# Performance work log

Hardware: AMD Instinct MI355X
Metric: run time of the kernel (lower is better)

The kernel has to match this reference:

```python
import jax, jax.numpy as jnp
import numpy as np

N_NODES = 128   # input_series_dim (nodes per graph)
FEAT = 512      # input_series_length
HID = 512       # hidden_channels
OUT = 10        # output_dimension
BATCH = 512     # batch_size


def setup_inputs() -> dict:
    key = jax.random.key(0)
    ks = jax.random.split(key, 9)
    s = 0.02
    x = jax.random.normal(ks[0], (BATCH, N_NODES, FEAT), jnp.float32)
    # dense_to_sparse(ones(N_NODES, N_NODES)) -> fully connected incl. diagonal,
    # row-major order, covering only nodes 0..N_NODES-1 (faithful to source).
    r = jnp.repeat(jnp.arange(N_NODES, dtype=jnp.int32), N_NODES)
    c = jnp.tile(jnp.arange(N_NODES, dtype=jnp.int32), N_NODES)
    edge_index = jnp.stack([r, c])  # (2, N_NODES**2)
    batch = jnp.repeat(jnp.arange(BATCH, dtype=jnp.int32), N_NODES)  # (BATCH*N_NODES,)
    W1 = jax.random.normal(ks[1], (FEAT, HID), jnp.float32) * s
    b1 = jnp.zeros((HID,), jnp.float32)
    W2 = jax.random.normal(ks[2], (HID, HID), jnp.float32) * s
    b2 = jnp.zeros((HID,), jnp.float32)
    W3 = jax.random.normal(ks[3], (HID, HID), jnp.float32) * s
    b3 = jnp.zeros((HID,), jnp.float32)
    Wlin = jax.random.normal(ks[4], (HID, OUT), jnp.float32) * s
    blin = jnp.zeros((OUT,), jnp.float32)
    return {"x": x, "W1": W1, "b1": b1, "W2": W2, "b2": b2, "W3": W3,
            "b3": b3, "Wlin": Wlin, "blin": blin,
            "edge_index": edge_index, "batch": batch}


def gcn_conv(h, src, dst, W, b):
    # PyG GCNConv: linear transform, add self-loops for ALL N nodes, symmetric norm,
    # scatter-add aggregate at dst, add bias.
    N = h.shape[0]
    h = h @ W
    loop = jnp.arange(N, dtype=src.dtype)
    s = jnp.concatenate([src, loop])
    d = jnp.concatenate([dst, loop])
    deg = jax.ops.segment_sum(jnp.ones(s.shape[0], h.dtype), d, num_segments=N)
    dinv = jnp.where(deg > 0, jax.lax.rsqrt(deg), jnp.zeros((), h.dtype))
    norm = dinv[s] * dinv[d]                     # (E+N,)
    out = jax.ops.segment_sum(norm[:, None] * h[s], d, num_segments=N)
    return out + b


def reference(x, W1, b1, W2, b2, W3, b3, Wlin, blin, edge_index, batch):
    x = x.reshape(-1, x.shape[-1]).astype(jnp.float32)   # (B*N_NODES, FEAT)
    src, dst = edge_index[0], edge_index[1]
    h = jax.nn.relu(gcn_conv(x, src, dst, W1, b1))
    h = jax.nn.relu(gcn_conv(h, src, dst, W2, b2))
    h = gcn_conv(h, src, dst, W3, b3)                    # layers == 3 path
    B = BATCH
    sums = jax.ops.segment_sum(h, batch, num_segments=B)
    cnt = jax.ops.segment_sum(jnp.ones((h.shape[0],), h.dtype), batch, num_segments=B)
    pooled = sums / cnt[:, None]                         # global_mean_pool
    # dropout p=0.5 is identity in eval mode
    return pooled @ Wlin + blin                          # (BATCH, OUT)
```

## Files before the change

### kernel.cpp

```cpp
#include <hip/hip_runtime.h>
#include <hip/hip_bf16.h>


typedef __attribute__((ext_vector_type(8))) short short8;
typedef __attribute__((ext_vector_type(4))) float f32x4;
typedef __attribute__((ext_vector_type(2))) unsigned int uint2v;

#define AS_G __attribute__((address_space(1)))
#define AS_L __attribute__((address_space(3)))

__device__ __forceinline__ void gload_lds16(const void* g, void* l) {
  __builtin_amdgcn_global_load_lds((const AS_G void*)g, (AS_L void*)l, 16, 0, 0);
}

__device__ __forceinline__ unsigned int pack2_bf16(float a, float b) {
  unsigned int ua = __float_as_uint(a);
  unsigned int ub = __float_as_uint(b);
  ua += 0x7FFFu + ((ua >> 16) & 1u);
  ub += 0x7FFFu + ((ub >> 16) & 1u);
  return (ua >> 16) | (ub & 0xFFFF0000u);
}

__device__ __forceinline__ unsigned short bf16_rne(float a) {
  unsigned int ua = __float_as_uint(a);
  ua += 0x7FFFu + ((ua >> 16) & 1u);
  return (unsigned short)(ua >> 16);
}

__global__ __launch_bounds__(1024) void fused_gcn(
    const float* __restrict__ x,
    const __hip_bfloat16* __restrict__ W1t,
    const __hip_bfloat16* __restrict__ W2t,
    const float* __restrict__ b1,
    const float* __restrict__ b2,
    float* __restrict__ P)
{
  __shared__ __align__(16) __hip_bfloat16 smem[81920];

  const int t  = threadIdx.x;
  const int g  = blockIdx.x;
  const int wave = t >> 6;
  const int l    = t & 63;
  const int q    = l >> 4;
  const int r16  = l & 15;
  const int wm   = (wave & 1) * 64;
  const int wn   = (wave >> 1) * 64;

  const int arow = t >> 3;
  const int kq   = t & 7;
  const float* ga = x + ((size_t)g * 128 + arow) * 512 + kq * 4;
  const int awoff = arow * 32 + (((kq >> 1) ^ ((arow >> 1) & 3)) << 3) + (kq & 1) * 4;

  const int brow = t >> 2;
  const int bgc  = (t & 3) ^ ((brow >> 1) & 3);
  const size_t boff = (size_t)brow * 512 + bgc * 8;
  const __hip_bfloat16* g1b0 = W1t + boff;
  const __hip_bfloat16* g1b1 = g1b0 + (size_t)256 * 512;

  f32x4 acc[4][4];
#pragma unroll
  for (int i = 0; i < 4; ++i)
#pragma unroll
    for (int j = 0; j < 4; ++j)
      acc[i][j] = (f32x4)0.0f;

  {
    f32x4 a0 = *(const f32x4*)(const void*)ga;
    gload_lds16(g1b0, smem + 49152 + wave * 512);
    gload_lds16(g1b1, smem + 49152 + 8192 + wave * 512);
    uint2v w;
    w[0] = pack2_bf16(a0[0], a0[1]);
    w[1] = pack2_bf16(a0[2], a0[3]);
    *(uint2v*)(void*)(smem + awoff) = w;
  }
  for (int kt = 0; kt < 16; ++kt) {
    const int cur = kt & 1;
    const int nxt = cur ^ 1;
    __syncthreads();

    f32x4 aN;
    if (kt < 15) {
      const int ko = (kt + 1) * 32;
      aN = *(const f32x4*)(const void*)(ga + ko);
      gload_lds16(g1b0 + ko, smem + 49152 + nxt * 16384 + wave * 512);
      gload_lds16(g1b1 + ko, smem + 49152 + nxt * 16384 + 8192 + wave * 512);
    }

    short8 af[4], bfr[4];
#pragma unroll
    for (int i = 0; i < 4; ++i) {
      const int row = wm + i * 16 + r16;
      const int c   = (q ^ ((row >> 1) & 3)) << 3;
      af[i] = *(const short8*)(const void*)(smem + cur * 4096 + row * 32 + c);
    }
#pragma unroll
    for (int j = 0; j < 4; ++j) {
      const int row = wn + j * 16 + r16;
      const int c   = (q ^ ((row >> 1) & 3)) << 3;
      bfr[j] = *(const short8*)(const void*)(smem + 49152 + cur * 16384 + row * 32 + c);
    }
#pragma unroll
    for (int i = 0; i < 4; ++i)
#pragma unroll
      for (int j = 0; j < 4; ++j)
        acc[i][j] = __builtin_amdgcn_mfma_f32_16x16x32_bf16(af[i], bfr[j], acc[i][j], 0, 0, 0);

    if (kt < 15) {
      uint2v w;
      w[0] = pack2_bf16(aN[0], aN[1]);
      w[1] = pack2_bf16(aN[2], aN[3]);
      *(uint2v*)(void*)(smem + nxt * 4096 + awoff) = w;
    }
  }
  __syncthreads();

  float* redf = (float*)(smem + 65536);
  float* Sbuf = (float*)(smem + 67584);

  if (g == 0) {
    float sj[4];
#pragma unroll
    for (int j = 0; j < 4; ++j) {
      float a = 0.0f;
#pragma unroll
      for (int i = 0; i < 4; ++i)
#pragma unroll
        for (int r = 0; r < 4; ++r)
          a += acc[i][j][r];
      a += __shfl_xor(a, 16, 64);
      a += __shfl_xor(a, 32, 64);
      sj[j] = a;
    }
    if (q == 0) {
#pragma unroll
      for (int j = 0; j < 4; ++j) redf[wave * 64 + j * 16 + r16] = sj[j];
    }
    __syncthreads();
    if (t < 512)
      Sbuf[t] = redf[((t >> 6) * 2) * 64 + (t & 63)] +
                redf[((t >> 6) * 2 + 1) * 64 + (t & 63)];
    __syncthreads();
#pragma unroll
    for (int j = 0; j < 4; ++j) {
      const int col = wn + j * 16 + r16;
      const float bv = b1[col];
      const float Sv = Sbuf[col];
#pragma unroll
      for (int i = 0; i < 4; ++i)
#pragma unroll
        for (int r = 0; r < 4; ++r) {
          const int row = wm + i * 16 + q * 4 + r;
          const float v = fmaxf((Sv + acc[i][j][r]) * (1.0f / 129.0f) + bv, 0.0f);
          const float o = __shfl_xor(v, 1, 64);
          if ((r16 & 1) == 0) {
            const int sl = (col >> 3) ^ (row & 7);
            *(unsigned int*)(void*)(smem + row * 512 + sl * 8 + (col & 7)) = pack2_bf16(v, o);
          }
        }
    }
  } else {
#pragma unroll
    for (int j = 0; j < 4; ++j) {
      const int col = wn + j * 16 + r16;
      const float bv = b1[col];
#pragma unroll
      for (int i = 0; i < 4; ++i)
#pragma unroll
        for (int r = 0; r < 4; ++r) {
          const int row = wm + i * 16 + q * 4 + r;
          const float v = fmaxf(acc[i][j][r] + bv, 0.0f);
          const float o = __shfl_xor(v, 1, 64);
          if ((r16 & 1) == 0) {
            const int sl = (col >> 3) ^ (row & 7);
            *(unsigned int*)(void*)(smem + row * 512 + sl * 8 + (col & 7)) = pack2_bf16(v, o);
          }
        }
    }
  }

#pragma unroll
  for (int i = 0; i < 4; ++i)
#pragma unroll
    for (int j = 0; j < 4; ++j)
      acc[i][j] = (f32x4)0.0f;

  const __hip_bfloat16* g2b0 = W2t + boff;
  const __hip_bfloat16* g2b1 = g2b0 + (size_t)256 * 512;

  for (int kt = 0; kt < 16; ++kt) {
    __syncthreads();
    const int ko = kt * 32;
    gload_lds16(g2b0 + ko, smem + 65536 + wave * 512);
    gload_lds16(g2b1 + ko, smem + 65536 + 8192 + wave * 512);
    __syncthreads();

    short8 af[4], bfr[4];
#pragma unroll
    for (int i = 0; i < 4; ++i) {
      const int row = wm + i * 16 + r16;
      const int sl  = (kt * 4 + q) ^ (row & 7);
      af[i] = *(const short8*)(const void*)(smem + row * 512 + sl * 8);
    }
#pragma unroll
    for (int j = 0; j < 4; ++j) {
      const int row = wn + j * 16 + r16;
      const int c   = (q ^ ((row >> 1) & 3)) << 3;
      bfr[j] = *(const short8*)(const void*)(smem + 65536 + row * 32 + c);
    }
#pragma unroll
    for (int i = 0; i < 4; ++i)
#pragma unroll
      for (int j = 0; j < 4; ++j)
        acc[i][j] = __builtin_amdgcn_mfma_f32_16x16x32_bf16(af[i], bfr[j], acc[i][j], 0, 0, 0);
  }
  __syncthreads();

  float pj[4];
  if (g == 0) {
    float sj[4];
#pragma unroll
    for (int j = 0; j < 4; ++j) {
      float a = 0.0f;
#pragma unroll
      for (int i = 0; i < 4; ++i)
#pragma unroll
        for (int r = 0; r < 4; ++r)
          a += acc[i][j][r];
      a += __shfl_xor(a, 16, 64);
      a += __shfl_xor(a, 32, 64);
      sj[j] = a;
    }
    if (q == 0) {
#pragma unroll
      for (int j = 0; j < 4; ++j) redf[wave * 64 + j * 16 + r16] = sj[j];
    }
    __syncthreads();
    if (t < 512)
      Sbuf[t] = redf[((t >> 6) * 2) * 64 + (t & 63)] +
                redf[((t >> 6) * 2 + 1) * 64 + (t & 63)];
    __syncthreads();
#pragma unroll
    for (int j = 0; j < 4; ++j) {
      const float bv = b2[wn + j * 16 + r16];
      const float Sv = Sbuf[wn + j * 16 + r16];
      float a = 0.0f;
#pragma unroll
      for (int i = 0; i < 4; ++i)
#pragma unroll
        for (int r = 0; r < 4; ++r)
          a += fmaxf((Sv + acc[i][j][r]) * (1.0f / 129.0f) + bv, 0.0f);
      a += __shfl_xor(a, 16, 64);
      a += __shfl_xor(a, 32, 64);
      pj[j] = a;
    }
  } else {
#pragma unroll
    for (int j = 0; j < 4; ++j) {
      const float bv = b2[wn + j * 16 + r16];
      float a = 0.0f;
#pragma unroll
      for (int i = 0; i < 4; ++i)
#pragma unroll
        for (int r = 0; r < 4; ++r)
          a += fmaxf(acc[i][j][r] + bv, 0.0f);
      a += __shfl_xor(a, 16, 64);
      a += __shfl_xor(a, 32, 64);
      pj[j] = a;
    }
  }
  if (q == 0) {
#pragma unroll
    for (int j = 0; j < 4; ++j) redf[wave * 64 + j * 16 + r16] = pj[j];
  }
  __syncthreads();
  if (t < 512)
    P[(size_t)g * 512 + t] =
        (redf[((t >> 6) * 2) * 64 + (t & 63)] +
         redf[((t >> 6) * 2 + 1) * 64 + (t & 63)]) * (1.0f / 128.0f);
}

__global__ void fold_w(const float* __restrict__ W3,
                       const float* __restrict__ Wlin,
                       const float* __restrict__ b3,
                       const float* __restrict__ blin,
                       float* __restrict__ Wf, float* __restrict__ bfv) {
  const int c = blockIdx.x;
  const int l = threadIdx.x;
  float acc[10];
#pragma unroll
  for (int o = 0; o < 10; ++o) acc[o] = 0.0f;
  for (int n = l; n < 512; n += 64) {
    const float wv = W3[c * 512 + n];
#pragma unroll
    for (int o = 0; o < 10; ++o) acc[o] += wv * Wlin[n * 10 + o];
  }
#pragma unroll
  for (int off = 32; off; off >>= 1)
#pragma unroll
    for (int o = 0; o < 10; ++o) acc[o] += __shfl_down(acc[o], off, 64);
  if (l == 0) {
#pragma unroll
    for (int o = 0; o < 10; ++o) Wf[c * 10 + o] = acc[o];
  }
  if (c < 10) {
    float s = 0.0f;
    for (int k = l; k < 512; k += 64) s += b3[k] * Wlin[k * 10 + c];
#pragma unroll
    for (int off = 32; off; off >>= 1) s += __shfl_down(s, off, 64);
    if (l == 0) bfv[c] = s + blin[c];
  }
}

__global__ void final_out(const float* __restrict__ P,
                          const float* __restrict__ Wf,
                          const float* __restrict__ bfv,
                          float* __restrict__ out) {
  const int m = blockIdx.x;
  const int l = threadIdx.x;
  float acc[10];
#pragma unroll
  for (int o = 0; o < 10; ++o) acc[o] = 0.0f;
  for (int c = l; c < 512; c += 64) {
    const float p = P[m * 512 + c];
#pragma unroll
    for (int o = 0; o < 10; ++o) acc[o] += p * Wf[c * 10 + o];
  }
#pragma unroll
  for (int off = 32; off; off >>= 1)
#pragma unroll
    for (int o = 0; o < 10; ++o) acc[o] += __shfl_down(acc[o], off, 64);
  if (l == 0) {
#pragma unroll
    for (int o = 0; o < 10; ++o) out[m * 10 + o] = acc[o] + bfv[o];
  }
}

__global__ void transpose512x2(const float* __restrict__ Wa,
                               const float* __restrict__ Wb,
                               unsigned short* __restrict__ Wat,
                               unsigned short* __restrict__ Wbt) {
  const float* W = blockIdx.z ? Wb : Wa;
  unsigned short* Wt = blockIdx.z ? Wbt : Wat;
  __shared__ float tile[32][33];
  const int tx = threadIdx.x, ty = threadIdx.y;
  tile[ty][tx] = W[(blockIdx.y * 32 + ty) * 512 + blockIdx.x * 32 + tx];
  __syncthreads();
  Wt[(blockIdx.x * 32 + ty) * 512 + blockIdx.y * 32 + tx] = bf16_rne(tile[tx][ty]);
}

extern "C" void kernel_launch(void* const* d_in, const int* in_sizes, int n_in,
                              void* d_out, int out_size, void* d_ws, size_t ws_size,
                              hipStream_t stream) {
  const float* x    = (const float*)d_in[0];
  const float* W1   = (const float*)d_in[1];
  const float* b1   = (const float*)d_in[2];
  const float* W2   = (const float*)d_in[3];
  const float* b2   = (const float*)d_in[4];
  const float* W3   = (const float*)d_in[5];
  const float* b3   = (const float*)d_in[6];
  const float* Wlin = (const float*)d_in[7];
  const float* blin = (const float*)d_in[8];
  float* out = (float*)d_out;

  char* ws = (char*)d_ws;
  unsigned short* W1t = (unsigned short*)ws;
  unsigned short* W2t = W1t + 512 * 512;
  float* P            = (float*)(W2t + 512 * 512);
  float* Wf           = P + 512 * 512;
  float* bfv          = Wf + 512 * 10;

  transpose512x2<<<dim3(16, 16, 2), dim3(32, 32), 0, stream>>>(W1, W2, W1t, W2t);
  fold_w<<<512, 64, 0, stream>>>(W3, Wlin, b3, blin, Wf, bfv);

  fused_gcn<<<512, 1024, 0, stream>>>(
      x, (const __hip_bfloat16*)W1t, (const __hip_bfloat16*)W2t, b1, b2, P);

  final_out<<<512, 64, 0, stream>>>(P, Wf, bfv, out);
}
```

Measured before the change: 289.7 us.

## Pipeline layer-2 weight loads with staggered waves and fuse head and prep kernels

The layer-2 GEMM loop now splits each B tile load into two halves loaded at different points. Waves 0-7 compute on the first half while the second half streams in, then waves 8-15 compute while the next first half is prefetched, with s_setprio raised around the MFMA bursts. The final 512x10 projection is folded into the tail of fused_gcn, which removes the P round-trip and the final_out launch. The transpose and fold_w kernels are merged into one prep launch. This cuts the number of kernel launches and barrier-bound stalls, but the half-split schedule depends on LDS buffer timing and wave ordering holding up.

```diff
diff --git a/kernel.cpp b/kernel.cpp
--- a/kernel.cpp
+++ b/kernel.cpp
@@ -33,7 +33,9 @@
     const __hip_bfloat16* __restrict__ W2t,
     const float* __restrict__ b1,
     const float* __restrict__ b2,
-    float* __restrict__ P)
+    const float* __restrict__ Wf,
+    const float* __restrict__ bfv,
+    float* __restrict__ out)
 {
   __shared__ __align__(16) __hip_bfloat16 smem[81920];
 
@@ -114,8 +116,12 @@
   }
   __syncthreads();
 
-  float* redf = (float*)(smem + 65536);
-  float* Sbuf = (float*)(smem + 67584);
+  const __hip_bfloat16* g2b0 = W2t + boff;
+  const __hip_bfloat16* g2b1 = g2b0 + (size_t)256 * 512;
+  gload_lds16(g2b0, smem + 65536 + wave * 512);
+
+  float* redf = (float*)(smem + 73728);
+  float* Sbuf = (float*)(smem + 75776);
 
   if (g == 0) {
     float sj[4];
@@ -184,34 +190,56 @@
     for (int j = 0; j < 4; ++j)
       acc[i][j] = (f32x4)0.0f;
 
-  const __hip_bfloat16* g2b0 = W2t + boff;
-  const __hip_bfloat16* g2b1 = g2b0 + (size_t)256 * 512;
-
   for (int kt = 0; kt < 16; ++kt) {
     __syncthreads();
-    const int ko = kt * 32;
-    gload_lds16(g2b0 + ko, smem + 65536 + wave * 512);
-    gload_lds16(g2b1 + ko, smem + 65536 + 8192 + wave * 512);
-    __syncthreads();
-
-    short8 af[4], bfr[4];
-#pragma unroll
-    for (int i = 0; i < 4; ++i) {
-      const int row = wm + i * 16 + r16;
-      const int sl  = (kt * 4 + q) ^ (row & 7);
-      af[i] = *(const short8*)(const void*)(smem + row * 512 + sl * 8);
-    }
-#pragma unroll
-    for (int j = 0; j < 4; ++j) {
-      const int row = wn + j * 16 + r16;
-      const int c   = (q ^ ((row >> 1) & 3)) << 3;
-      bfr[j] = *(const short8*)(const void*)(smem + 65536 + row * 32 + c);
-    }
-#pragma unroll
-    for (int i = 0; i < 4; ++i)
-#pragma unroll
-      for (int j = 0; j < 4; ++j)
-        acc[i][j] = __builtin_amdgcn_mfma_f32_16x16x32_bf16(af[i], bfr[j], acc[i][j], 0, 0, 0);
+    gload_lds16(g2b1 + kt * 32, smem + 73728 + wave * 512);
+    if (wave < 8) {
+      short8 af[4], bfr[4];
+#pragma unroll
+      for (int i = 0; i < 4; ++i) {
+        const int row = wm + i * 16 + r16;
+        const int sl  = (kt * 4 + q) ^ (row & 7);
+        af[i] = *(const short8*)(const void*)(smem + row * 512 + sl * 8);
+      }
+#pragma unroll
+      for (int j = 0; j < 4; ++j) {
+        const int row = wn + j * 16 + r16;
+        const int c   = (q ^ ((row >> 1) & 3)) << 3;
+        bfr[j] = *(const short8*)(const void*)(smem + 65536 + row * 32 + c);
+      }
+      __builtin_amdgcn_s_setprio(1);
+#pragma unroll
+      for (int i = 0; i < 4; ++i)
+#pragma unroll
+        for (int j = 0; j < 4; ++j)
+          acc[i][j] = __builtin_amdgcn_mfma_f32_16x16x32_bf16(af[i], bfr[j], acc[i][j], 0, 0, 0);
+      __builtin_amdgcn_s_setprio(0);
+    }
+    __syncthreads();
+    if (kt < 15)
+      gload_lds16(g2b0 + (kt + 1) * 32, smem + 65536 + wave * 512);
+    if (wave >= 8) {
+      short8 af[4], bfr[4];
+#pragma unroll
+      for (int i = 0; i < 4; ++i) {
+        const int row = wm + i * 16 + r16;
+        const int sl  = (kt * 4 + q) ^ (row & 7);
+        af[i] = *(const short8*)(const void*)(smem + row * 512 + sl * 8);
+      }
+#pragma unroll
+      for (int j = 0; j < 4; ++j) {
+        const int row = wn + j * 16 + r16;
+        const int c   = (q ^ ((row >> 1) & 3)) << 3;
+        bfr[j] = *(const short8*)(const void*)(smem + 65536 + row * 32 + c);
+      }
+      __builtin_amdgcn_s_setprio(1);
+#pragma unroll
+      for (int i = 0; i < 4; ++i)
+#pragma unroll
+        for (int j = 0; j < 4; ++j)
+          acc[i][j] = __builtin_amdgcn_mfma_f32_16x16x32_bf16(af[i], bfr[j], acc[i][j], 0, 0, 0);
+      __builtin_amdgcn_s_setprio(0);
+    }
   }
   __syncthreads();
 
@@ -274,78 +302,68 @@
   }
   __syncthreads();
   if (t < 512)
-    P[(size_t)g * 512 + t] =
+    Sbuf[t] =
         (redf[((t >> 6) * 2) * 64 + (t & 63)] +
          redf[((t >> 6) * 2 + 1) * 64 + (t & 63)]) * (1.0f / 128.0f);
-}
-
-__global__ void fold_w(const float* __restrict__ W3,
-                       const float* __restrict__ Wlin,
-                       const float* __restrict__ b3,
-                       const float* __restrict__ blin,
-                       float* __restrict__ Wf, float* __restrict__ bfv) {
-  const int c = blockIdx.x;
-  const int l = threadIdx.x;
-  float acc[10];
-#pragma unroll
-  for (int o = 0; o < 10; ++o) acc[o] = 0.0f;
-  for (int n = l; n < 512; n += 64) {
-    const float wv = W3[c * 512 + n];
-#pragma unroll
-    for (int o = 0; o < 10; ++o) acc[o] += wv * Wlin[n * 10 + o];
-  }
-#pragma unroll
-  for (int off = 32; off; off >>= 1)
-#pragma unroll
-    for (int o = 0; o < 10; ++o) acc[o] += __shfl_down(acc[o], off, 64);
-  if (l == 0) {
-#pragma unroll
-    for (int o = 0; o < 10; ++o) Wf[c * 10 + o] = acc[o];
-  }
-  if (c < 10) {
+  __syncthreads();
+
+  if (wave < 10) {
     float s = 0.0f;
-    for (int k = l; k < 512; k += 64) s += b3[k] * Wlin[k * 10 + c];
+    for (int c = l; c < 512; c += 64) s += Sbuf[c] * Wf[c * 10 + wave];
 #pragma unroll
     for (int off = 32; off; off >>= 1) s += __shfl_down(s, off, 64);
-    if (l == 0) bfv[c] = s + blin[c];
-  }
-}
-
-__global__ void final_out(const float* __restrict__ P,
-                          const float* __restrict__ Wf,
-                          const float* __restrict__ bfv,
-                          float* __restrict__ out) {
-  const int m = blockIdx.x;
-  const int l = threadIdx.x;
-  float acc[10];
-#pragma unroll
-  for (int o = 0; o < 10; ++o) acc[o] = 0.0f;
-  for (int c = l; c < 512; c += 64) {
-    const float p = P[m * 512 + c];
-#pragma unroll
-    for (int o = 0; o < 10; ++o) acc[o] += p * Wf[c * 10 + o];
-  }
-#pragma unroll
-  for (int off = 32; off; off >>= 1)
-#pragma unroll
-    for (int o = 0; o < 10; ++o) acc[o] += __shfl_down(acc[o], off, 64);
-  if (l == 0) {
-#pragma unroll
-    for (int o = 0; o < 10; ++o) out[m * 10 + o] = acc[o] + bfv[o];
-  }
-}
-
-__global__ void transpose512x2(const float* __restrict__ Wa,
-                               const float* __restrict__ Wb,
-                               unsigned short* __restrict__ Wat,
-                               unsigned short* __restrict__ Wbt) {
-  const float* W = blockIdx.z ? Wb : Wa;
-  unsigned short* Wt = blockIdx.z ? Wbt : Wat;
-  __shared__ float tile[32][33];
-  const int tx = threadIdx.x, ty = threadIdx.y;
-  tile[ty][tx] = W[(blockIdx.y * 32 + ty) * 512 + blockIdx.x * 32 + tx];
-  __syncthreads();
-  Wt[(blockIdx.x * 32 + ty) * 512 + blockIdx.y * 32 + tx] = bf16_rne(tile[tx][ty]);
+    if (l == 0) out[(size_t)g * 10 + wave] = s + bfv[wave];
+  }
+}
+
+__global__ __launch_bounds__(1024) void prep(
+    const float* __restrict__ W1, const float* __restrict__ W2,
+    unsigned short* __restrict__ W1t, unsigned short* __restrict__ W2t,
+    const float* __restrict__ W3, const float* __restrict__ Wlin,
+    const float* __restrict__ b3, const float* __restrict__ blin,
+    float* __restrict__ Wf, float* __restrict__ bfv) {
+  const int b = blockIdx.x;
+  if (b < 512) {
+    __shared__ float tile[32][33];
+    const int z  = b >> 8;
+    const int by = (b >> 4) & 15;
+    const int bx = b & 15;
+    const float* W = z ? W2 : W1;
+    unsigned short* Wt = z ? W2t : W1t;
+    const int tx = threadIdx.x & 31;
+    const int ty = threadIdx.x >> 5;
+    tile[ty][tx] = W[(by * 32 + ty) * 512 + bx * 32 + tx];
+    __syncthreads();
+    Wt[(bx * 32 + ty) * 512 + by * 32 + tx] = bf16_rne(tile[tx][ty]);
+  } else {
+    const int c = b - 512;
+    const int l = threadIdx.x;
+    if (l < 64) {
+      float acc[10];
+#pragma unroll
+      for (int o = 0; o < 10; ++o) acc[o] = 0.0f;
+      for (int n = l; n < 512; n += 64) {
+        const float wv = W3[c * 512 + n];
+#pragma unroll
+        for (int o = 0; o < 10; ++o) acc[o] += wv * Wlin[n * 10 + o];
+      }
+#pragma unroll
+      for (int off = 32; off; off >>= 1)
+#pragma unroll
+        for (int o = 0; o < 10; ++o) acc[o] += __shfl_down(acc[o], off, 64);
+      if (l == 0) {
+#pragma unroll
+        for (int o = 0; o < 10; ++o) Wf[c * 10 + o] = acc[o];
+      }
+      if (c < 10) {
+        float s = 0.0f;
+        for (int k = l; k < 512; k += 64) s += b3[k] * Wlin[k * 10 + c];
+#pragma unroll
+        for (int off = 32; off; off >>= 1) s += __shfl_down(s, off, 64);
+        if (l == 0) bfv[c] = s + blin[c];
+      }
+    }
+  }
 }
 
 extern "C" void kernel_launch(void* const* d_in, const int* in_sizes, int n_in,
@@ -365,15 +383,11 @@
   char* ws = (char*)d_ws;
   unsigned short* W1t = (unsigned short*)ws;
   unsigned short* W2t = W1t + 512 * 512;
-  float* P            = (float*)(W2t + 512 * 512);
-  float* Wf           = P + 512 * 512;
+  float* Wf           = (float*)(W2t + 512 * 512);
   float* bfv          = Wf + 512 * 10;
 
-  transpose512x2<<<dim3(16, 16, 2), dim3(32, 32), 0, stream>>>(W1, W2, W1t, W2t);
-  fold_w<<<512, 64, 0, stream>>>(W3, Wlin, b3, blin, Wf, bfv);
+  prep<<<1024, 1024, 0, stream>>>(W1, W2, W1t, W2t, W3, Wlin, b3, blin, Wf, bfv);
 
   fused_gcn<<<512, 1024, 0, stream>>>(
-      x, (const __hip_bfloat16*)W1t, (const __hip_bfloat16*)W2t, b1, b2, P);
-
-  final_out<<<512, 64, 0, stream>>>(P, Wf, bfv, out);
-}
+      x, (const __hip_bfloat16*)W1t, (const __hip_bfloat16*)W2t, b1, b2, Wf, bfv, out);
+}
```

Result: faster. 277.4 us (-4.2%).
